# Kernel tuning notes

Hardware: AMD Instinct MI355X
Metric: run time of the kernel (lower is better)

The kernel has to match this reference:

```python
import jax, jax.numpy as jnp
import numpy as np

N_EVENTS = 4096
TS_SIZE = 1024
N_NEURONS = 64
LAMBDA_HOMEO = 0.25
HOMEO_FLAG = True


def setup_inputs() -> dict:
    key = jax.random.key(0)
    k1, k2 = jax.random.split(key)
    all_ts = jax.random.normal(k1, (N_EVENTS, TS_SIZE), dtype=jnp.float32)
    # torch.nn.init.uniform_(weight, a=0, b=1)
    W = jax.random.uniform(k2, (N_NEURONS, TS_SIZE), dtype=jnp.float32)
    cumhisto = jnp.ones((N_NEURONS,), dtype=jnp.float32)
    return {"all_ts": all_ts, "W": W, "cumhisto": cumhisto, "clustering_flag": 1}


def reference(all_ts, W, cumhisto, clustering_flag):
    n_neurons = W.shape[0]
    if clustering_flag:
        # Sequential online competitive learning: per event, normalize, score,
        # argmax winner, update the winner's codebook row and its histogram.
        def step(carry, ts):
            Wc, hist = carry
            ts = ts / jnp.linalg.norm(ts)
            w_norm = jnp.linalg.norm(Wc, axis=1)          # [n_neurons]
            beta = (Wc @ ts) / w_norm                      # [n_neurons]
            if HOMEO_FLAG:
                gain = jnp.exp(LAMBDA_HOMEO * (1.0 - n_neurons * hist / hist.sum()))
                scores = gain * beta
            else:
                scores = beta
            n_star = jnp.argmax(scores)
            Ck = Wc[n_star]                                # [ts_size]
            alpha = 0.01 / (1.0 + hist[n_star] / 20000.0)
            Wc = Wc.at[n_star].set(Ck + alpha * beta[n_star] * (ts - Ck))
            hist = hist.at[n_star].add(1.0)
            return (Wc, hist), n_star

        (_, _), n_star = jax.lax.scan(step, (W, cumhisto), all_ts)
        return n_star  # [n_events] int winners
    else:
        # NB: original normalizes over dim=0 (the event dim) — faithful to source.
        x = all_ts.reshape(all_ts.shape[0], -1)
        x = x / jnp.linalg.norm(x, axis=0)
        beta = (x @ W.T) / jnp.linalg.norm(W, axis=1)      # [n_events, n_neurons]
        return jnp.argmax(beta, axis=1)
```

## Files before the change

### kernel.cpp

```cpp
#include <hip/hip_runtime.h>
#include <math.h>

#define N_EVENTS 4096
#define TS 1024
#define NN 64
#define BLK 512
#define NBLK (N_EVENTS / BLK)

typedef int v2i __attribute__((ext_vector_type(2)));

template<int CTRL>
__device__ __forceinline__ float dppmov(float x) {
    return __int_as_float(__builtin_amdgcn_mov_dpp(__float_as_int(x), CTRL, 0xF, 0xF, true));
}

#if __has_builtin(__builtin_amdgcn_permlane16_swap) && __has_builtin(__builtin_amdgcn_permlane32_swap)
__device__ __forceinline__ void sswap16(float x, float& a, float& b) {
    v2i r = __builtin_amdgcn_permlane16_swap(__float_as_int(x), __float_as_int(x), false, false);
    a = __int_as_float(r[0]); b = __int_as_float(r[1]);
}
__device__ __forceinline__ void sswap32(float x, float& a, float& b) {
    v2i r = __builtin_amdgcn_permlane32_swap(__float_as_int(x), __float_as_int(x), false, false);
    a = __int_as_float(r[0]); b = __int_as_float(r[1]);
}
#else
__device__ __forceinline__ void sswap16(float x, float& a, float& b) {
    asm("v_mov_b32 %0, %2\n\tv_mov_b32 %1, %2\n\ts_nop 1\n\tv_permlane16_swap_b32 %0, %1"
        : "=&v"(a), "=&v"(b) : "v"(x));
}
__device__ __forceinline__ void sswap32(float x, float& a, float& b) {
    asm("v_mov_b32 %0, %2\n\tv_mov_b32 %1, %2\n\ts_nop 1\n\tv_permlane32_swap_b32 %0, %1"
        : "=&v"(a), "=&v"(b) : "v"(x));
}
#endif

__device__ __forceinline__ float wred_add(float x) {
    x += dppmov<0xB1>(x);
    x += dppmov<0x4E>(x);
    x += dppmov<0x141>(x);
    x += dppmov<0x140>(x);
    { float a, b; sswap16(x, a, b); x = a + b; }
    { float a, b; sswap32(x, a, b); x = a + b; }
    return x;
}
__device__ __forceinline__ float wred_max(float x) {
    x = fmaxf(x, dppmov<0xB1>(x));
    x = fmaxf(x, dppmov<0x4E>(x));
    x = fmaxf(x, dppmov<0x141>(x));
    x = fmaxf(x, dppmov<0x140>(x));
    { float a, b; sswap16(x, a, b); x = fmaxf(a, b); }
    { float a, b; sswap32(x, a, b); x = fmaxf(a, b); }
    return x;
}


__global__ void norms_kernel(const float* __restrict__ all_ts, float* __restrict__ nrm) {
    const int l = threadIdx.x & 63;
    const int wv = threadIdx.x >> 6;
    const int e = blockIdx.x * 4 + wv;
    const float4* src = (const float4*)(all_ts + (size_t)e * TS);
    float s = 0.f;
    #pragma unroll
    for (int c = 0; c < 4; ++c) {
        float4 f = src[64 * c + l];
        s = fmaf(f.x, f.x, fmaf(f.y, f.y, fmaf(f.z, f.z, fmaf(f.w, f.w, s))));
    }
    const float tsn = sqrtf(wred_add(s));
    if (l == 0) nrm[e] = tsn;
}

__global__ void wnorm0_kernel(const float* __restrict__ W, const float* __restrict__ ch,
                              float* __restrict__ wn_g, float* __restrict__ hist_g) {
    const int l = threadIdx.x & 63;
    const int wv = threadIdx.x >> 6;
    const int r = blockIdx.x * 4 + wv;
    const float4* row = (const float4*)(W + (size_t)r * TS);
    float s = 0.f;
    #pragma unroll
    for (int c = 0; c < 4; ++c) {
        float4 f = row[64 * c + l];
        s = fmaf(f.x, f.x, fmaf(f.y, f.y, fmaf(f.z, f.z, fmaf(f.w, f.w, s))));
    }
    const float tot = wred_add(s);
    if (l == 0) wn_g[r] = sqrtf(tot);
    if (blockIdx.x == 0 && threadIdx.x < NN) hist_g[threadIdx.x] = ch[threadIdx.x];
}

__global__ void gtile_kernel(const float* __restrict__ ts, float* __restrict__ Gt) {
    const int tj = blockIdx.x, ti = blockIdx.y, b = blockIdx.z;
    if (tj < ti) return;
    __shared__ float As[32][36];
    __shared__ float Bs[32][36];
    const float* base = ts + (size_t)b * BLK * TS;
    const int tid = threadIdx.x;
    const int ty = tid >> 4, tx = tid & 15;
    const int lr = tid >> 3, lc = (tid & 7) << 2;
    float a00 = 0, a01 = 0, a10 = 0, a11 = 0;
    for (int k0 = 0; k0 < TS; k0 += 32) {
        float4 av = *(const float4*)(base + (size_t)(ti * 32 + lr) * TS + k0 + lc);
        float4 bv = *(const float4*)(base + (size_t)(tj * 32 + lr) * TS + k0 + lc);
        __syncthreads();
        *(float4*)&As[lr][lc] = av;
        *(float4*)&Bs[lr][lc] = bv;
        __syncthreads();
        #pragma unroll
        for (int kk = 0; kk < 32; kk += 4) {
            const float4 x0 = *(const float4*)&As[2 * ty][kk];
            const float4 x1 = *(const float4*)&As[2 * ty + 1][kk];
            const float4 y0 = *(const float4*)&Bs[2 * tx][kk];
            const float4 y1 = *(const float4*)&Bs[2 * tx + 1][kk];
            a00 = fmaf(x0.x, y0.x, fmaf(x0.y, y0.y, fmaf(x0.z, y0.z, fmaf(x0.w, y0.w, a00))));
            a01 = fmaf(x0.x, y1.x, fmaf(x0.y, y1.y, fmaf(x0.z, y1.z, fmaf(x0.w, y1.w, a01))));
            a10 = fmaf(x1.x, y0.x, fmaf(x1.y, y0.y, fmaf(x1.z, y0.z, fmaf(x1.w, y0.w, a10))));
            a11 = fmaf(x1.x, y1.x, fmaf(x1.y, y1.y, fmaf(x1.z, y1.z, fmaf(x1.w, y1.w, a11))));
        }
    }
    float* g = Gt + (size_t)b * BLK * BLK;
    const int i0 = ti * 32 + 2 * ty, j0 = tj * 32 + 2 * tx;
    g[(size_t)i0 * BLK + j0]           = a00;
    g[(size_t)i0 * BLK + j0 + 1]       = a01;
    g[(size_t)(i0 + 1) * BLK + j0]     = a10;
    g[(size_t)(i0 + 1) * BLK + j0 + 1] = a11;
}

__global__ void dgemm_kernel(const float* __restrict__ Wc, const float* __restrict__ tsb,
                             float* __restrict__ D_g) {
    const int tj = blockIdx.x, ti = blockIdx.y;
    __shared__ float As[32][36];
    __shared__ float Bs[32][36];
    const int tid = threadIdx.x;
    const int ty = tid >> 4, tx = tid & 15;
    const int lr = tid >> 3, lc = (tid & 7) << 2;
    float a00 = 0, a01 = 0, a10 = 0, a11 = 0;
    for (int k0 = 0; k0 < TS; k0 += 32) {
        float4 av = *(const float4*)(Wc + (size_t)(ti * 32 + lr) * TS + k0 + lc);
        float4 bv = *(const float4*)(tsb + (size_t)(tj * 32 + lr) * TS + k0 + lc);
        __syncthreads();
        *(float4*)&As[lr][lc] = av;
        *(float4*)&Bs[lr][lc] = bv;
        __syncthreads();
        #pragma unroll
        for (int kk = 0; kk < 32; kk += 4) {
            const float4 x0 = *(const float4*)&As[2 * ty][kk];
            const float4 x1 = *(const float4*)&As[2 * ty + 1][kk];
            const float4 y0 = *(const float4*)&Bs[2 * tx][kk];
            const float4 y1 = *(const float4*)&Bs[2 * tx + 1][kk];
            a00 = fmaf(x0.x, y0.x, fmaf(x0.y, y0.y, fmaf(x0.z, y0.z, fmaf(x0.w, y0.w, a00))));
            a01 = fmaf(x0.x, y1.x, fmaf(x0.y, y1.y, fmaf(x0.z, y1.z, fmaf(x0.w, y1.w, a01))));
            a10 = fmaf(x1.x, y0.x, fmaf(x1.y, y0.y, fmaf(x1.z, y0.z, fmaf(x1.w, y0.w, a10))));
            a11 = fmaf(x1.x, y1.x, fmaf(x1.y, y1.y, fmaf(x1.z, y1.z, fmaf(x1.w, y1.w, a11))));
        }
    }
    const int n0 = ti * 32 + 2 * ty, f0 = tj * 32 + 2 * tx;
    D_g[(size_t)f0 * 64       + ((n0)     ^ (f0 & 31))]       = a00;
    D_g[(size_t)(f0 + 1) * 64 + ((n0)     ^ ((f0 + 1) & 31))] = a01;
    D_g[(size_t)f0 * 64       + ((n0 + 1) ^ (f0 & 31))]       = a10;
    D_g[(size_t)(f0 + 1) * 64 + ((n0 + 1) ^ ((f0 + 1) & 31))] = a11;
}

__global__ void rebuild_kernel(float* __restrict__ Wc, const float* __restrict__ ts,
                               const int* __restrict__ win, const float* __restrict__ coef_g,
                               const float* __restrict__ nrm, int b) {
    const int n = blockIdx.x;
    const int d = blockIdx.y * 256 + threadIdx.x;
    float wv = Wc[(size_t)n * TS + d];
    const int e0 = b * BLK;
    #pragma unroll 1
    for (int i = 0; i < BLK; ++i) {
        if (win[e0 + i] == n) {
            const float rtn = __builtin_amdgcn_rcpf(nrm[e0 + i]);
            const float tn = ts[(size_t)(e0 + i) * TS + d] * rtn;
            const float c = coef_g[e0 + i];
            wv = fmaf(c, tn - wv, wv);
        }
    }
    Wc[(size_t)n * TS + d] = wv;
}

#define DUMPB 131072u

#define STEP(I, GC, TSC, SDC)                                                   \
    {                                                                           \
        const float tsn = TSC;                                                  \
        const float sd  = SDC;                                                  \
        TSC = nrm[e0 + (I) + 2];                     \
        SDC = Gt_b[513 * ((I) + 2) + 1];                                        \
        const float rtn  = __builtin_amdgcn_rcpf(tsn);                          \
        const float beta = dv * __builtin_amdgcn_rcpf(tsn * wnl);               \
        const float score = gain * beta;                                        \
        const float coefl = alpha * beta;                                       \
                   \
        const float dv_pre = Dl[((((I) + 1) & 511) << 6) + (l ^ (((I) + 1) & 31))]; \
        const float smax = wred_max(score);                                     \
        const unsigned long long mk = __ballot(score == smax);                  \
        const int ns = (int)(__ffsll(mk) - 1);                                  \
        const float coef = __shfl(coefl, ns, 64);                               \
        const float bw   = __shfl(beta,  ns, 64);                               \
        if (l == 0) { out[e0 + (I)] = ns; coef_g[e0 + (I)] = coef; }            \
              \
        {                                                                       \
            const unsigned f0u = (unsigned)((I) + 1 + l);                       \
            const unsigned fb = (f0u << 8) + (((unsigned)ns ^ (f0u & 31u)) << 2); \
            const unsigned dmp = DUMPB + ((unsigned)l << 2);                    \
            _Pragma("unroll")                                                   \
            for (int k = 0; k < 8; ++k) {                                       \
                unsigned a = fb + 16384u * (unsigned)k;                         \
                a = a < dmp ? a : dmp;                                          \
                float* p = (float*)((char*)Dl + a);                             \
                const float dvv = *p;                                           \
                *p = fmaf(coef, rtn * GC[k] - dvv, dvv);                        \
            }                                                                   \
        }                                                                       \
                                  \
        {                                                                       \
            const float* gr = Gt_b + 512 * ((I) + 2) + ((I) + 3 + l);           \
            _Pragma("unroll")                                                   \
            for (int k = 0; k < 8; ++k) GC[k] = gr[64 * k];                     \
        }                                                                       \
             \
        const float fx = fmaf(coef, rtn * sd - dv_pre, dv_pre);                 \
        dv = (l == ns) ? fx : dv_pre;                                           \
        const float om = 1.0f - coef;                                           \
        const float wn_new = sqrtf(om * om * wnl * wnl                          \
                                   + 2.0f * coef * om * bw * wnl + coef * coef); \
        if (l == ns) { wnl = wn_new; hll += 1.0f; }                             \
        hs += 1.0f;                                                             \
        gain  = __expf(0.25f - 16.0f * hll * __builtin_amdgcn_rcpf(hs));        \
        alpha = 0.01f * __builtin_amdgcn_rcpf(fmaf(hll, 1.0f / 20000.0f, 1.0f)); \
    }

__launch_bounds__(64, 1)
__global__ void seq_kernel(const float* __restrict__ D_g, const float* __restrict__ Gt_b,
                           const float* __restrict__ nrm, float* __restrict__ wn_g,
                           float* __restrict__ hist_g, int* __restrict__ out,
                           float* __restrict__ coef_g, int b)
{
    __shared__ float Dl[NN * BLK + 64];
    const int l = threadIdx.x;

    {
        const float4* Dg4 = (const float4*)D_g;
        float4* Dl4 = (float4*)Dl;
        #pragma unroll 8
        for (int c = 0; c < 128; ++c) Dl4[c * 64 + l] = Dg4[c * 64 + l];
    }

    const int e0 = b * BLK;
    float wnl = wn_g[l];
    float hll = hist_g[l];
    float hs  = 64.0f + (float)e0;
    float gain  = __expf(0.25f - 16.0f * hll * __builtin_amdgcn_rcpf(hs));
    float alpha = 0.01f * __builtin_amdgcn_rcpf(fmaf(hll, 1.0f / 20000.0f, 1.0f));

    float gA[8], gB[8];
    {
        const float* gr = Gt_b + (1 + l);
        #pragma unroll
        for (int k = 0; k < 8; ++k) gA[k] = gr[64 * k];
    }
    {
        const float* gr = Gt_b + 512 + (2 + l);
        #pragma unroll
        for (int k = 0; k < 8; ++k) gB[k] = gr[64 * k];
    }
    float tsA = nrm[e0], tsB = nrm[e0 + 1];
    float sdA = Gt_b[1], sdB = Gt_b[513 + 1];
    float dv = Dl[l];

    #pragma unroll 1
    for (int i = 0; i < BLK; i += 2) {
        STEP(i,     gA, tsA, sdA);
        STEP(i + 1, gB, tsB, sdB);
    }

    wn_g[l] = wnl;
    hist_g[l] = hll;
}

#define GT_OFF    0
#define NRM_OFF   2097152
#define WN_OFF    2101248
#define HIST_OFF  2101312
#define COEF_OFF  2101376
#define D_OFF     2105472
#define W_OFF     2138240

extern "C" void kernel_launch(void* const* d_in, const int* in_sizes, int n_in,
                              void* d_out, int out_size, void* d_ws, size_t ws_size,
                              hipStream_t stream) {
    const float* all_ts   = (const float*)d_in[0];
    const float* W        = (const float*)d_in[1];
    const float* cumhisto = (const float*)d_in[2];
    int* out = (int*)d_out;
    float* ws = (float*)d_ws;

    float* Gt     = ws + GT_OFF;
    float* nrm    = ws + NRM_OFF;
    float* wn_g   = ws + WN_OFF;
    float* hist_g = ws + HIST_OFF;
    float* coef_g = ws + COEF_OFF;
    float* D_g    = ws + D_OFF;
    float* W_cur  = ws + W_OFF;

    hipMemcpyAsync(W_cur, W, (size_t)NN * TS * sizeof(float),
                   hipMemcpyDeviceToDevice, stream);
    norms_kernel<<<N_EVENTS / 4, 256, 0, stream>>>(all_ts, nrm);
    wnorm0_kernel<<<16, 256, 0, stream>>>(W, cumhisto, wn_g, hist_g);
    gtile_kernel<<<dim3(16, 16, NBLK), 256, 0, stream>>>(all_ts, Gt);

    for (int b = 0; b < NBLK; ++b) {
        dgemm_kernel<<<dim3(16, 2), 256, 0, stream>>>(
            W_cur, all_ts + (size_t)b * BLK * TS, D_g);
        seq_kernel<<<1, 64, 0, stream>>>(
            D_g, Gt + (size_t)b * BLK * BLK, nrm, wn_g, hist_g, out, coef_g, b);
        if (b < NBLK - 1)
            rebuild_kernel<<<dim3(NN, 4), 256, 0, stream>>>(
                W_cur, all_ts, out, coef_g, nrm, b);
    }
}
```

Before: 2.922 ms.

## Speculate next-step argmax with top-two scores and a single-winner fixup

The sequential winner-selection loop is restructured. Each step now precomputes the next event's scores along with the top-two maxima, so the argmax only has to correct the one neuron changed by the previous update instead of doing a full wave reduction on the critical path. Norms are tracked as squared values with rsq, and per-lane state is fetched with readlane instead of shuffles. The seq kernel loads its LDS tile with 512 threads before dropping to one wave, rebuild stages winners, coefficients and reciprocal norms in shared memory, and the two norm kernels are merged into one launch. The speculative top-two logic adds complexity and depends on exact float equality to break ties correctly.

```diff
diff --git a/kernel.cpp b/kernel.cpp
--- a/kernel.cpp
+++ b/kernel.cpp
@@ -1,5 +1,6 @@
 #include <hip/hip_runtime.h>
 #include <math.h>
+#include <float.h>
 
 #define N_EVENTS 4096
 #define TS 1024
@@ -53,37 +54,44 @@
     return x;
 }
 
-
-__global__ void norms_kernel(const float* __restrict__ all_ts, float* __restrict__ nrm) {
+__device__ __forceinline__ float rdlane(float x, int lane) {
+    return __int_as_float(__builtin_amdgcn_readlane(__float_as_int(x), lane));
+}
+__device__ __forceinline__ float rdfirst(float x) {
+    return __int_as_float(__builtin_amdgcn_readfirstlane(__float_as_int(x)));
+}
+
+
+__global__ void prep_kernel(const float* __restrict__ all_ts, const float* __restrict__ W,
+                            const float* __restrict__ ch, float* __restrict__ nrm,
+                            float* __restrict__ wnsq_g, float* __restrict__ hist_g) {
     const int l = threadIdx.x & 63;
     const int wv = threadIdx.x >> 6;
-    const int e = blockIdx.x * 4 + wv;
-    const float4* src = (const float4*)(all_ts + (size_t)e * TS);
-    float s = 0.f;
-    #pragma unroll
-    for (int c = 0; c < 4; ++c) {
-        float4 f = src[64 * c + l];
-        s = fmaf(f.x, f.x, fmaf(f.y, f.y, fmaf(f.z, f.z, fmaf(f.w, f.w, s))));
-    }
-    const float tsn = sqrtf(wred_add(s));
-    if (l == 0) nrm[e] = tsn;
-}
-
-__global__ void wnorm0_kernel(const float* __restrict__ W, const float* __restrict__ ch,
-                              float* __restrict__ wn_g, float* __restrict__ hist_g) {
-    const int l = threadIdx.x & 63;
-    const int wv = threadIdx.x >> 6;
-    const int r = blockIdx.x * 4 + wv;
-    const float4* row = (const float4*)(W + (size_t)r * TS);
-    float s = 0.f;
-    #pragma unroll
-    for (int c = 0; c < 4; ++c) {
-        float4 f = row[64 * c + l];
-        s = fmaf(f.x, f.x, fmaf(f.y, f.y, fmaf(f.z, f.z, fmaf(f.w, f.w, s))));
-    }
-    const float tot = wred_add(s);
-    if (l == 0) wn_g[r] = sqrtf(tot);
-    if (blockIdx.x == 0 && threadIdx.x < NN) hist_g[threadIdx.x] = ch[threadIdx.x];
+    const int blk = blockIdx.x;
+    if (blk < 1024) {
+        const int e = blk * 4 + wv;
+        const float4* src = (const float4*)(all_ts + (size_t)e * TS);
+        float s = 0.f;
+        #pragma unroll
+        for (int c = 0; c < 4; ++c) {
+            float4 f = src[64 * c + l];
+            s = fmaf(f.x, f.x, fmaf(f.y, f.y, fmaf(f.z, f.z, fmaf(f.w, f.w, s))));
+        }
+        const float tsn = sqrtf(wred_add(s));
+        if (l == 0) nrm[e] = tsn;
+    } else {
+        const int r = (blk - 1024) * 4 + wv;
+        const float4* row = (const float4*)(W + (size_t)r * TS);
+        float s = 0.f;
+        #pragma unroll
+        for (int c = 0; c < 4; ++c) {
+            float4 f = row[64 * c + l];
+            s = fmaf(f.x, f.x, fmaf(f.y, f.y, fmaf(f.z, f.z, fmaf(f.w, f.w, s))));
+        }
+        const float tot = wred_add(s);
+        if (l == 0) wnsq_g[r] = tot;
+        if (blk == 1024 && threadIdx.x < NN) hist_g[threadIdx.x] = ch[threadIdx.x];
+    }
 }
 
 __global__ void gtile_kernel(const float* __restrict__ ts, float* __restrict__ Gt) {
@@ -161,97 +169,135 @@
 __global__ void rebuild_kernel(float* __restrict__ Wc, const float* __restrict__ ts,
                                const int* __restrict__ win, const float* __restrict__ coef_g,
                                const float* __restrict__ nrm, int b) {
+    __shared__ int   wl[BLK];
+    __shared__ float cl[BLK];
+    __shared__ float rl[BLK];
     const int n = blockIdx.x;
     const int d = blockIdx.y * 256 + threadIdx.x;
+    const int e0 = b * BLK;
+    for (int i = threadIdx.x; i < BLK; i += 256) {
+        wl[i] = win[e0 + i];
+        cl[i] = coef_g[e0 + i];
+        rl[i] = __builtin_amdgcn_rcpf(nrm[e0 + i]);
+    }
+    __syncthreads();
     float wv = Wc[(size_t)n * TS + d];
-    const int e0 = b * BLK;
-    #pragma unroll 1
+    #pragma unroll 4
     for (int i = 0; i < BLK; ++i) {
-        if (win[e0 + i] == n) {
-            const float rtn = __builtin_amdgcn_rcpf(nrm[e0 + i]);
-            const float tn = ts[(size_t)(e0 + i) * TS + d] * rtn;
-            const float c = coef_g[e0 + i];
-            wv = fmaf(c, tn - wv, wv);
+        if (wl[i] == n) {
+            const float tn = ts[(size_t)(e0 + i) * TS + d] * rl[i];
+            wv = fmaf(cl[i], tn - wv, wv);
         }
     }
     Wc[(size_t)n * TS + d] = wv;
 }
 
-#define DUMPB 131072u
-
-#define STEP(I, GC, TSC, SDC)                                                   \
+
+#define ITER(I, GC, TSC, TSO)                                                   \
     {                                                                           \
-        const float tsn = TSC;                                                  \
-        const float sd  = SDC;                                                  \
-        TSC = nrm[e0 + (I) + 2];                     \
-        SDC = Gt_b[513 * ((I) + 2) + 1];                                        \
-        const float rtn  = __builtin_amdgcn_rcpf(tsn);                          \
-        const float beta = dv * __builtin_amdgcn_rcpf(tsn * wnl);               \
-        const float score = gain * beta;                                        \
-        const float coefl = alpha * beta;                                       \
-                   \
-        const float dv_pre = Dl[((((I) + 1) & 511) << 6) + (l ^ (((I) + 1) & 31))]; \
-        const float smax = wred_max(score);                                     \
-        const unsigned long long mk = __ballot(score == smax);                  \
-        const int ns = (int)(__ffsll(mk) - 1);                                  \
-        const float coef = __shfl(coefl, ns, 64);                               \
-        const float bw   = __shfl(beta,  ns, 64);                               \
-        if (l == 0) { out[e0 + (I)] = ns; coef_g[e0 + (I)] = coef; }            \
-              \
+               \
+        const unsigned c1 = (unsigned)((I) + 1) & 511u;                         \
+        const float dv_nx = Dl[(c1 << 6) + ((unsigned)l ^ (c1 & 31u))];         \
+        const float rtn = rtncur;                                               \
+        float rg[8];                                                            \
+        _Pragma("unroll")                                                       \
+        for (int k = 0; k < 8; ++k) rg[k] = rtn * GC[k];                        \
+                        \
+        const float dvp   = rdlane(dvpre_carry, mprev);                         \
+        const float dvfix = fmaf(coef_prev, rgsd_prev - dvp, dvp);              \
+        const float bfix  = dvfix * rtn * rdlane(rwn, mprev);                   \
+        const float sfix  = rdlane(gain, mprev) * bfix;                         \
+        const float excl  = (m1 == (1ull << mprev)) ? v2 : v1;                  \
+        const float smax  = fmaxf(excl, sfix);                                  \
+        const float scorr = (l == mprev) ? sfix : s_carry;                      \
+        const unsigned long long bal = __ballot(scorr == smax);                 \
+        const int m = (int)(__ffsll(bal) - 1);                                  \
+        const float Dm   = (m == mprev) ? dvfix : rdlane(dvpre_carry, m);       \
+        const float betw = (m == mprev) ? bfix  : rdlane(beta_carry, m);        \
+        const float coef = rdlane(alpha, m) * betw;                             \
+        if (l == 0) { out[e0 + (I)] = m; coef_g[e0 + (I)] = coef; }             \
+                      \
         {                                                                       \
-            const unsigned f0u = (unsigned)((I) + 1 + l);                       \
-            const unsigned fb = (f0u << 8) + (((unsigned)ns ^ (f0u & 31u)) << 2); \
-            const unsigned dmp = DUMPB + ((unsigned)l << 2);                    \
+            const unsigned f0 = (unsigned)((I) + 1 + l) & 511u;                 \
+            const unsigned xr = ((unsigned)(m ^ (int)(f0 & 31u))) << 2;         \
             _Pragma("unroll")                                                   \
             for (int k = 0; k < 8; ++k) {                                       \
-                unsigned a = fb + 16384u * (unsigned)k;                         \
-                a = a < dmp ? a : dmp;                                          \
-                float* p = (float*)((char*)Dl + a);                             \
-                const float dvv = *p;                                           \
-                *p = fmaf(coef, rtn * GC[k] - dvv, dvv);                        \
+                const unsigned fk = ((f0 + 64u * (unsigned)k) & 511u) << 8;     \
+                float* p = (float*)((char*)Dl + (fk + xr));                     \
+                const float d0 = *p;                                            \
+                *p = fmaf(coef, rg[k] - d0, d0);                                \
             }                                                                   \
         }                                                                       \
-                                  \
+          \
+        const float wsq_m = rdlane(wnsq, m);                                    \
+        const float om = 1.0f - coef;                                           \
+        const float bwt = Dm * rtn;                                             \
+        const float wsq_new = fmaf(om * om, wsq_m,                              \
+                                   fmaf(2.0f * coef * om, bwt, coef * coef));   \
+        const float rwn_new = __builtin_amdgcn_rsqf(wsq_new);                   \
+        const float hll_new = rdlane(hll, m) + 1.0f;                            \
+        const float alp_new = 0.01f * __builtin_amdgcn_rcpf(fmaf(hll_new, 1.0f / 20000.0f, 1.0f)); \
+        if (l == m) { wnsq = wsq_new; rwn = rwn_new; hll = hll_new; alpha = alp_new; } \
+        hs += 1.0f;                                                             \
+        gain = __expf(0.25f - 16.0f * hll * __builtin_amdgcn_rcpf(hs));         \
+          \
+        const float rtn_nx = __builtin_amdgcn_rcpf(TSO);                        \
+        const float bst = dv_nx * rtn_nx * rwn;                                 \
+        const float sst = gain * bst;                                           \
+        v1 = wred_max(sst);                                                     \
+        m1 = __ballot(sst == v1);                                               \
+        v2 = wred_max((sst == v1) ? -FLT_MAX : sst);                            \
+        s_carry = sst; beta_carry = bst; dvpre_carry = dv_nx;                   \
+        mprev = m; coef_prev = coef;                                            \
+        rgsd_prev = rdfirst(rg[0]);              \
+        rtncur = rtn_nx;                                                        \
+                                         \
+        TSC = nrm[e0 + (I) + 2];                                                \
         {                                                                       \
             const float* gr = Gt_b + 512 * ((I) + 2) + ((I) + 3 + l);           \
             _Pragma("unroll")                                                   \
             for (int k = 0; k < 8; ++k) GC[k] = gr[64 * k];                     \
         }                                                                       \
-             \
-        const float fx = fmaf(coef, rtn * sd - dv_pre, dv_pre);                 \
-        dv = (l == ns) ? fx : dv_pre;                                           \
-        const float om = 1.0f - coef;                                           \
-        const float wn_new = sqrtf(om * om * wnl * wnl                          \
-                                   + 2.0f * coef * om * bw * wnl + coef * coef); \
-        if (l == ns) { wnl = wn_new; hll += 1.0f; }                             \
-        hs += 1.0f;                                                             \
-        gain  = __expf(0.25f - 16.0f * hll * __builtin_amdgcn_rcpf(hs));        \
-        alpha = 0.01f * __builtin_amdgcn_rcpf(fmaf(hll, 1.0f / 20000.0f, 1.0f)); \
-    }
-
-__launch_bounds__(64, 1)
+    }
+
+__launch_bounds__(512, 1)
 __global__ void seq_kernel(const float* __restrict__ D_g, const float* __restrict__ Gt_b,
-                           const float* __restrict__ nrm, float* __restrict__ wn_g,
+                           const float* __restrict__ nrm, float* __restrict__ wnsq_g,
                            float* __restrict__ hist_g, int* __restrict__ out,
                            float* __restrict__ coef_g, int b)
 {
-    __shared__ float Dl[NN * BLK + 64];
-    const int l = threadIdx.x;
+    __shared__ float Dl[NN * BLK];
+    const int t = threadIdx.x;
 
     {
         const float4* Dg4 = (const float4*)D_g;
         float4* Dl4 = (float4*)Dl;
-        #pragma unroll 8
-        for (int c = 0; c < 128; ++c) Dl4[c * 64 + l] = Dg4[c * 64 + l];
-    }
+        #pragma unroll
+        for (int c = 0; c < 16; ++c) Dl4[c * 512 + t] = Dg4[c * 512 + t];
+    }
+    __syncthreads();
+    if (t >= 64) return;
+    const int l = t;
 
     const int e0 = b * BLK;
-    float wnl = wn_g[l];
-    float hll = hist_g[l];
-    float hs  = 64.0f + (float)e0;
-    float gain  = __expf(0.25f - 16.0f * hll * __builtin_amdgcn_rcpf(hs));
+    float wnsq = wnsq_g[l];
+    float hll  = hist_g[l];
+    float rwn  = __builtin_amdgcn_rsqf(wnsq);
     float alpha = 0.01f * __builtin_amdgcn_rcpf(fmaf(hll, 1.0f / 20000.0f, 1.0f));
-
+    float hs = 64.0f + (float)e0;
+    float gain = __expf(0.25f - 16.0f * hll * __builtin_amdgcn_rcpf(hs));
+
+    float rtncur = __builtin_amdgcn_rcpf(nrm[e0]);
+    float dvpre_carry = Dl[l];
+    float beta_carry = dvpre_carry * rtncur * rwn;
+    float s_carry = gain * beta_carry;
+    float v1 = wred_max(s_carry);
+    unsigned long long m1 = __ballot(s_carry == v1);
+    float v2 = wred_max((s_carry == v1) ? -FLT_MAX : s_carry);
+    int mprev = 0;
+    float coef_prev = 0.0f, rgsd_prev = 0.0f;
+
+    float tsA = nrm[e0], tsB = nrm[e0 + 1];
     float gA[8], gB[8];
     {
         const float* gr = Gt_b + (1 + l);
@@ -263,17 +309,14 @@
         #pragma unroll
         for (int k = 0; k < 8; ++k) gB[k] = gr[64 * k];
     }
-    float tsA = nrm[e0], tsB = nrm[e0 + 1];
-    float sdA = Gt_b[1], sdB = Gt_b[513 + 1];
-    float dv = Dl[l];
 
     #pragma unroll 1
     for (int i = 0; i < BLK; i += 2) {
-        STEP(i,     gA, tsA, sdA);
-        STEP(i + 1, gB, tsB, sdB);
-    }
-
-    wn_g[l] = wnl;
+        ITER(i,     gA, tsA, tsB);
+        ITER(i + 1, gB, tsB, tsA);
+    }
+
+    wnsq_g[l] = wnsq;
     hist_g[l] = hll;
 }
 
@@ -296,7 +339,7 @@
 
     float* Gt     = ws + GT_OFF;
     float* nrm    = ws + NRM_OFF;
-    float* wn_g   = ws + WN_OFF;
+    float* wnsq_g = ws + WN_OFF;
     float* hist_g = ws + HIST_OFF;
     float* coef_g = ws + COEF_OFF;
     float* D_g    = ws + D_OFF;
@@ -304,15 +347,14 @@
 
     hipMemcpyAsync(W_cur, W, (size_t)NN * TS * sizeof(float),
                    hipMemcpyDeviceToDevice, stream);
-    norms_kernel<<<N_EVENTS / 4, 256, 0, stream>>>(all_ts, nrm);
-    wnorm0_kernel<<<16, 256, 0, stream>>>(W, cumhisto, wn_g, hist_g);
+    prep_kernel<<<1040, 256, 0, stream>>>(all_ts, W, cumhisto, nrm, wnsq_g, hist_g);
     gtile_kernel<<<dim3(16, 16, NBLK), 256, 0, stream>>>(all_ts, Gt);
 
     for (int b = 0; b < NBLK; ++b) {
         dgemm_kernel<<<dim3(16, 2), 256, 0, stream>>>(
             W_cur, all_ts + (size_t)b * BLK * TS, D_g);
-        seq_kernel<<<1, 64, 0, stream>>>(
-            D_g, Gt + (size_t)b * BLK * BLK, nrm, wn_g, hist_g, out, coef_g, b);
+        seq_kernel<<<1, 512, 0, stream>>>(
+            D_g, Gt + (size_t)b * BLK * BLK, nrm, wnsq_g, hist_g, out, coef_g, b);
         if (b < NBLK - 1)
             rebuild_kernel<<<dim3(NN, 4), 256, 0, stream>>>(
                 W_cur, all_ts, out, coef_g, nrm, b);
```

Result: slower. 3.217 ms (+10.1%).
